# Optimization experiments

Hardware: AMD Instinct MI355X
Metric: run time of the kernel (lower is better)

## Reference

```python
import jax, jax.numpy as jnp
import numpy as np

DIM = 96
HEADS = 6
HEAD_DIM = DIM // HEADS  # 16
WIN = 8
N = WIN * WIN            # 64
C = 4 * DIM              # 384
TABLE = (2 * WIN - 1) ** 2  # 225


def setup_inputs() -> dict:
    key = jax.random.key(0)
    ks = jax.random.split(key, 12)
    B_ = 2048  # num_windows * batch = 1024 * 2
    NW = 1024
    x = jax.random.normal(ks[0], (B_, N, C), dtype=jnp.float32)
    cross_x = jax.random.normal(ks[1], (B_, N, C), dtype=jnp.float32)
    rpi = jax.random.randint(ks[2], (N, N), 0, TABLE)
    mask = jnp.zeros((NW, N, N), dtype=jnp.float32)
    s = 0.02
    Wq = jax.random.normal(ks[3], (C, DIM), dtype=jnp.float32) * s
    bq = jnp.zeros((DIM,), dtype=jnp.float32)
    Wk = jax.random.normal(ks[4], (C, DIM), dtype=jnp.float32) * s
    bk = jnp.zeros((DIM,), dtype=jnp.float32)
    Wv = jax.random.normal(ks[5], (C, C), dtype=jnp.float32) * s
    bv = jnp.zeros((C,), dtype=jnp.float32)
    Wp = jax.random.normal(ks[6], (C, C), dtype=jnp.float32) * s
    bp = jnp.zeros((C,), dtype=jnp.float32)
    rpb_table = jax.random.normal(ks[7], (TABLE, HEADS), dtype=jnp.float32) * 0.02
    return {"x": x, "cross_x": cross_x, "rpi": rpi, "mask": mask,
            "Wq": Wq, "bq": bq, "Wk": Wk, "bk": bk, "Wv": Wv, "bv": bv,
            "Wp": Wp, "bp": bp, "rpb_table": rpb_table}


def reference(x, cross_x, rpi, mask, Wq, bq, Wk, bk, Wv, bv, Wp, bp, rpb_table):
    b_, n, c = x.shape
    scale = HEAD_DIM ** (-0.5)
    # projections: q,k -> dim; v -> c (=4*dim)
    q = (x @ Wq + bq).reshape(b_, n, HEADS, HEAD_DIM).transpose(0, 2, 1, 3)
    k = (cross_x @ Wk + bk).reshape(b_, n, HEADS, HEAD_DIM).transpose(0, 2, 1, 3)
    v = (cross_x @ Wv + bv).reshape(b_, n, HEADS, c // HEADS).transpose(0, 2, 1, 3)
    attn = jnp.einsum('bhnd,bhmd->bhnm', q * scale, k)
    # relative position bias: gather (n*n,) indices -> (n, n, heads) -> (heads, n, n)
    bias = rpb_table[rpi.reshape(-1)].reshape(n, n, HEADS).transpose(2, 0, 1)
    attn = attn + bias[None]
    nw = mask.shape[0]
    attn = attn.reshape(b_ // nw, nw, HEADS, n, n) + mask[None, :, None]
    attn = attn.reshape(b_, HEADS, n, n)
    attn = jax.nn.softmax(attn, axis=-1)
    out = jnp.einsum('bhnm,bhmd->bhnd', attn, v)  # (b_, heads, n, c//heads)
    out = out.transpose(0, 2, 1, 3).reshape(b_, n, c)
    out = out @ Wp + bp
    return out
```

## Files before the change

kernel.cpp:

```cpp
#include <hip/hip_runtime.h>
#include <hip/hip_bf16.h>


typedef __attribute__((ext_vector_type(8))) short short8;
typedef __attribute__((ext_vector_type(4))) float f32x4;

__device__ __forceinline__ f32x4 mfma_b16(short8 a, short8 b, f32x4 c) {
  return __builtin_amdgcn_mfma_f32_16x16x32_bf16(a, b, c, 0, 0, 0);
}

__device__ __forceinline__ unsigned short f2bf(float x) {
  return __builtin_bit_cast(unsigned short, __float2bfloat16(x));
}

__device__ __forceinline__ unsigned pack2(float a, float b) {
  return (unsigned)f2bf(a) | ((unsigned)f2bf(b) << 16);
}

__device__ __forceinline__ int swz48(int c, int r) {
  return (c & ~7) | ((c ^ r) & 7);
}

__device__ __forceinline__ void gl_lds16(const char* g, char* l) {
  __builtin_amdgcn_global_load_lds(
      (const __attribute__((address_space(1))) unsigned int*)g,
      (__attribute__((address_space(3))) unsigned int*)l, 16, 0, 0);
}

__global__ void prep_k(const float* __restrict__ Wq, const float* __restrict__ Wk,
                       const float* __restrict__ Wv, const float* __restrict__ Wp,
                       const float* __restrict__ rpb, const int* __restrict__ rpi,
                       const float* __restrict__ bk, const float* __restrict__ bv,
                       unsigned short* __restrict__ Wq_t, unsigned short* __restrict__ Wkv_t,
                       unsigned short* __restrict__ Wp_t, float* __restrict__ bias6,
                       float* __restrict__ bias_kv) {
  const int T0 = 96 * 384, T1 = 480 * 384, T2 = 384 * 384, T3 = 6 * 4096, T4 = 480;
  int total = T0 + T1 + T2 + T3 + T4;
  for (int i = blockIdx.x * blockDim.x + threadIdx.x; i < total;
       i += gridDim.x * blockDim.x) {
    int r = i;
    if (r < T0) {
      int n = r / 384, k = r % 384;
      Wq_t[r] = f2bf(Wq[k * 96 + n]);
    } else if ((r -= T0) < T1) {
      int n = r / 384, k = r % 384;
      Wkv_t[r] = f2bf(n < 96 ? Wk[k * 96 + n] : Wv[k * 384 + (n - 96)]);
    } else if ((r -= T1) < T2) {
      int n = r / 384, k = r % 384;
      Wp_t[r] = f2bf(Wp[k * 384 + n]);
    } else if ((r -= T2) < T3) {
      int h = r >> 12, ij = r & 4095;
      bias6[r] = rpb[rpi[ij] * 6 + h];
    } else {
      r -= T3;
      bias_kv[r] = (r < 96) ? bk[r] : bv[r - 96];
    }
  }
}

template <int A_MODE, int OUT_MODE, int NX>
__global__ __launch_bounds__(256, 4) void gemm3_k(
    const void* __restrict__ Av, const unsigned short* __restrict__ Bt,
    const float* __restrict__ bias, void* __restrict__ Outv,
    unsigned short* __restrict__ k_out, unsigned short* __restrict__ vt_out) {
  __shared__ char lds[40960];
  constexpr int AB[2] = {0, 8192}, BB[2] = {16384, 28672};
  const int tid = threadIdx.x, lane = tid & 63, wid = tid >> 6;
  const int g = blockIdx.x;
  const int lg_id = (g & 7) * (NX * 256) + (g >> 3);
  const int my = lg_id / NX, nx = lg_id - my * NX;
  const int m0 = my * 64, n0 = nx * 96;
  const int wm = (wid >> 1) * 32, wn = (wid & 1) * 48;
  const int lr = lane & 15, lg = lane >> 4;

  float4 areg[4];
  const int ar = tid >> 2, aq = tid & 3;

  auto a_issue_f32 = [&](int kt) {
    const float* A = (const float*)Av + (size_t)(m0 + ar) * 384 + kt * 64 + aq * 16;
#pragma unroll
    for (int p = 0; p < 4; ++p) areg[p] = *reinterpret_cast<const float4*>(A + p * 4);
  };
  auto a_write_f32 = [&](char* Ab) {
    unsigned pk[8];
#pragma unroll
    for (int p = 0; p < 4; ++p) {
      pk[p * 2]     = pack2(areg[p].x, areg[p].y);
      pk[p * 2 + 1] = pack2(areg[p].z, areg[p].w);
    }
    const int c0 = aq * 2;
    *reinterpret_cast<uint4*>(Ab + ar * 128 + ((c0 ^ (ar & 7)) * 16)) =
        make_uint4(pk[0], pk[1], pk[2], pk[3]);
    *reinterpret_cast<uint4*>(Ab + ar * 128 + (((c0 + 1) ^ (ar & 7)) * 16)) =
        make_uint4(pk[4], pk[5], pk[6], pk[7]);
  };
  auto b_issue = [&](int kt, char* Bb) {
#pragma unroll
    for (int j = 0; j < 3; ++j) {
      const int rb = (wid * 3 + j) * 8;
      const int row = rb + (lane >> 3), c = lane & 7;
      gl_lds16((const char*)Bt + (size_t)(n0 + row) * 768 + kt * 128 +
                   ((c ^ (row & 7)) * 16),
               Bb + rb * 128);
    }
  };

  f32x4 acc[2][3];
#pragma unroll
  for (int i = 0; i < 2; ++i)
#pragma unroll
    for (int j = 0; j < 3; ++j) acc[i][j] = (f32x4){0.f, 0.f, 0.f, 0.f};

  a_issue_f32(0);
  a_write_f32(lds + AB[0]);
  b_issue(0, lds + BB[0]);
  __syncthreads();

  int cur = 0;
  for (int kt = 0; kt < 6; ++kt) {
    char* An = lds + AB[cur ^ 1];
    char* Bn = lds + BB[cur ^ 1];
    if (kt < 5) {
      a_issue_f32(kt + 1);
      b_issue(kt + 1, Bn);
    }
    {
      const char* Ab = lds + AB[cur];
      const char* Bb = lds + BB[cur];
#pragma unroll
      for (int ks = 0; ks < 2; ++ks) {
        short8 a[2], b[3];
#pragma unroll
        for (int mf = 0; mf < 2; ++mf) {
          const int row = wm + mf * 16 + lr;
          a[mf] = *reinterpret_cast<const short8*>(
              Ab + row * 128 + (((ks * 4 + lg) ^ (row & 7)) * 16));
        }
#pragma unroll
        for (int nf = 0; nf < 3; ++nf) {
          const int row = wn + nf * 16 + lr;
          b[nf] = *reinterpret_cast<const short8*>(
              Bb + row * 128 + (((ks * 4 + lg) ^ (row & 7)) * 16));
        }
#pragma unroll
        for (int mf = 0; mf < 2; ++mf)
#pragma unroll
          for (int nf = 0; nf < 3; ++nf)
            acc[mf][nf] = mfma_b16(a[mf], b[nf], acc[mf][nf]);
      }
    }
    if (kt < 5) a_write_f32(An);
    __syncthreads();
    cur ^= 1;
  }

  if (OUT_MODE == 0 || (OUT_MODE == 2 && nx == 0)) {
    unsigned short* dst = (OUT_MODE == 0) ? (unsigned short*)Outv : k_out;
#pragma unroll
    for (int mf = 0; mf < 2; ++mf)
#pragma unroll
      for (int nf = 0; nf < 3; ++nf) {
        const int col = wn + nf * 16 + lr;
        const float bb = bias[col];
#pragma unroll
        for (int r = 0; r < 4; ++r) {
          const int row = wm + mf * 16 + lg * 4 + r;
          *reinterpret_cast<unsigned short*>(lds + row * 208 + col * 2) =
              f2bf(acc[mf][nf][r] + bb);
        }
      }
    __syncthreads();
#pragma unroll
    for (int j = 0; j < 3; ++j) {
      const int Lb = (j * 256 + tid) * 16;
      const int row = Lb / 192, inner = Lb % 192;
      *reinterpret_cast<uint4*>((char*)dst + (size_t)(m0 + row) * 192 + inner) =
          *reinterpret_cast<const uint4*>(lds + row * 208 + inner);
    }
  } else {
#pragma unroll
    for (int mf = 0; mf < 2; ++mf)
#pragma unroll
      for (int nf = 0; nf < 3; ++nf) {
        const int dl = wn + nf * 16 + lr;
        const float bb = bias[n0 + dl];
        const int tok0 = wm + mf * 16 + lg * 4;
        *reinterpret_cast<unsigned*>(lds + dl * 144 + tok0 * 2) =
            pack2(acc[mf][nf][0] + bb, acc[mf][nf][1] + bb);
        *reinterpret_cast<unsigned*>(lds + dl * 144 + tok0 * 2 + 4) =
            pack2(acc[mf][nf][2] + bb, acc[mf][nf][3] + bb);
      }
    __syncthreads();
#pragma unroll
    for (int j = 0; j < 3; ++j) {
      const int Lc = j * 256 + tid;
      const int dl = Lc >> 3, c = Lc & 7;
      *reinterpret_cast<uint4*>((char*)vt_out + (size_t)my * 49152 +
                                (size_t)((nx - 1) * 96 + dl) * 128 +
                                ((c ^ (dl & 7)) << 4)) =
          *reinterpret_cast<const uint4*>(lds + dl * 144 + c * 16);
    }
  }
}

__global__ __launch_bounds__(256, 2) void ap_k(
    const unsigned short* __restrict__ q_buf, const unsigned short* __restrict__ k_buf,
    const unsigned short* __restrict__ vt_buf, const float* __restrict__ bias6,
    const float* __restrict__ mask, const unsigned short* __restrict__ Wp_t,
    const float* __restrict__ bp, float* __restrict__ out) {
  __shared__ char lds[81920];
  const int tid = threadIdx.x, lane = tid & 63, wid = tid >> 6;
  const int lr = lane & 15, lg = lane >> 4;
  const int w = blockIdx.x;

  auto b_issue = [&](int T, char* Bb) {
    const int nc = T / 6, kt = T - nc * 6;
#pragma unroll
    for (int j = 0; j < 3; ++j) {
      const int rb = (wid * 3 + j) * 8;
      const int row = rb + (lane >> 3), c = lane & 7;
      gl_lds16((const char*)Wp_t + (size_t)(nc * 96 + row) * 768 + kt * 128 +
                   ((c ^ (row & 7)) * 16),
               Bb + rb * 128);
    }
  };

  const char* vsrc = (const char*)vt_buf + (size_t)w * 49152;
#pragma unroll
  for (int j = 0; j < 12; ++j) {
    const int off = (wid * 12 + j) * 1024;
    gl_lds16(vsrc + off + lane * 16, lds + off);
  }
  b_issue(0, lds + 57344);
  b_issue(1, lds + 57344 + 12288);
  __syncthreads();

  unsigned stash[48];
  char* Plds = lds + 49152;
  const float* mw = mask + (size_t)(w & 1023) * 4096;
  const int iq = wid * 16 + lr;

  short8 qa_c = {0, 0, 0, 0, 0, 0, 0, 0};
  short8 kf_c[4];
  float4 bm_c[4];
#pragma unroll
  for (int tj = 0; tj < 4; ++tj) kf_c[tj] = (short8){0, 0, 0, 0, 0, 0, 0, 0};
  if (lg < 2) {
    qa_c = *reinterpret_cast<const short8*>(
        q_buf + (size_t)(w * 64 + iq) * 96 + lg * 8);
#pragma unroll
    for (int tj = 0; tj < 4; ++tj)
      kf_c[tj] = *reinterpret_cast<const short8*>(
          k_buf + (size_t)(w * 64 + tj * 16 + lr) * 96 + lg * 8);
  }
#pragma unroll
  for (int tj = 0; tj < 4; ++tj) {
    const int j0 = tj * 16 + lg * 4;
    const float4 bi = *reinterpret_cast<const float4*>(bias6 + iq * 64 + j0);
    const float4 mk = *reinterpret_cast<const float4*>(mw + iq * 64 + j0);
    bm_c[tj] = make_float4(bi.x + mk.x, bi.y + mk.y, bi.z + mk.z, bi.w + mk.w);
  }

#pragma unroll
  for (int h = 0; h < 6; ++h) {
    short8 qa_n = {0, 0, 0, 0, 0, 0, 0, 0};
    short8 kf_n[4];
    float4 bm_n[4];
#pragma unroll
    for (int tj = 0; tj < 4; ++tj) kf_n[tj] = (short8){0, 0, 0, 0, 0, 0, 0, 0};
    if (h < 5) {
      if (lg < 2) {
        qa_n = *reinterpret_cast<const short8*>(
            q_buf + (size_t)(w * 64 + iq) * 96 + (h + 1) * 16 + lg * 8);
#pragma unroll
        for (int tj = 0; tj < 4; ++tj)
          kf_n[tj] = *reinterpret_cast<const short8*>(
              k_buf + (size_t)(w * 64 + tj * 16 + lr) * 96 + (h + 1) * 16 + lg * 8);
      }
#pragma unroll
      for (int tj = 0; tj < 4; ++tj) {
        const int j0 = tj * 16 + lg * 4;
        const float4 bi = *reinterpret_cast<const float4*>(
            bias6 + (h + 1) * 4096 + iq * 64 + j0);
        const float4 mk = *reinterpret_cast<const float4*>(mw + iq * 64 + j0);
        bm_n[tj] = make_float4(bi.x + mk.x, bi.y + mk.y, bi.z + mk.z, bi.w + mk.w);
      }
    }

    float sv[4][4];
#pragma unroll
    for (int tj = 0; tj < 4; ++tj) {
      f32x4 z = {0.f, 0.f, 0.f, 0.f};
      f32x4 s = mfma_b16(kf_c[tj], qa_c, z);
      sv[tj][0] = s[0] * 0.25f + bm_c[tj].x;
      sv[tj][1] = s[1] * 0.25f + bm_c[tj].y;
      sv[tj][2] = s[2] * 0.25f + bm_c[tj].z;
      sv[tj][3] = s[3] * 0.25f + bm_c[tj].w;
    }
    float mx = sv[0][0];
#pragma unroll
    for (int tj = 0; tj < 4; ++tj)
#pragma unroll
      for (int r = 0; r < 4; ++r) mx = fmaxf(mx, sv[tj][r]);
    mx = fmaxf(mx, __shfl_xor(mx, 16));
    mx = fmaxf(mx, __shfl_xor(mx, 32));
    float sum = 0.f;
#pragma unroll
    for (int tj = 0; tj < 4; ++tj)
#pragma unroll
      for (int r = 0; r < 4; ++r) {
        sv[tj][r] = __expf(sv[tj][r] - mx);
        sum += sv[tj][r];
      }
    sum += __shfl_xor(sum, 16);
    sum += __shfl_xor(sum, 32);
    const float inv = 1.0f / sum;
#pragma unroll
    for (int tj = 0; tj < 4; ++tj) {
      const int c = tj * 2 + (lg >> 1);
      uint2 st;
      st.x = pack2(sv[tj][0] * inv, sv[tj][1] * inv);
      st.y = pack2(sv[tj][2] * inv, sv[tj][3] * inv);
      *reinterpret_cast<uint2*>(Plds + iq * 128 + ((c ^ (iq & 7)) << 4) +
                                (lg & 1) * 8) = st;
    }
    short8 pa[2];
#pragma unroll
    for (int ks = 0; ks < 2; ++ks)
      pa[ks] = *reinterpret_cast<const short8*>(
          Plds + iq * 128 + (((ks * 4 + lg) ^ (iq & 7)) << 4));
    __builtin_amdgcn_s_setprio(1);
#pragma unroll
    for (int td = 0; td < 4; ++td) {
      f32x4 o = {0.f, 0.f, 0.f, 0.f};
#pragma unroll
      for (int ks = 0; ks < 2; ++ks) {
        const int d = h * 64 + td * 16 + lr;
        short8 vb = *reinterpret_cast<const short8*>(
            lds + d * 128 + (((ks * 4 + lg) ^ (d & 7)) << 4));
        o = mfma_b16(vb, pa[ks], o);
      }
      stash[h * 8 + td * 2 + 0] = pack2(o[0], o[1]);
      stash[h * 8 + td * 2 + 1] = pack2(o[2], o[3]);
    }
    __builtin_amdgcn_s_setprio(0);
    qa_c = qa_n;
#pragma unroll
    for (int tj = 0; tj < 4; ++tj) {
      kf_c[tj] = kf_n[tj];
      bm_c[tj] = bm_n[tj];
    }
  }
  __syncthreads();

#pragma unroll
  for (int h = 0; h < 6; ++h)
#pragma unroll
    for (int td = 0; td < 4; ++td)
#pragma unroll
      for (int p2 = 0; p2 < 2; ++p2) {
        const int c0 = h * 64 + td * 16 + lg * 4 + p2 * 2;
        *reinterpret_cast<unsigned*>(
            lds + iq * 768 + swz48(c0 >> 3, iq) * 16 + ((c0 * 2) & 15)) =
            stash[h * 8 + td * 2 + p2];
      }
  __syncthreads();

  const int wm = (wid >> 1) * 32, wn = (wid & 1) * 48;
  f32x4 acc[2][3];
#pragma unroll
  for (int i = 0; i < 2; ++i)
#pragma unroll
    for (int j = 0; j < 3; ++j) acc[i][j] = (f32x4){0.f, 0.f, 0.f, 0.f};

#pragma unroll 1
  for (int T = 0; T < 24; ++T) {
    const int nc = T / 6, kt = T - nc * 6;
    if (T >= 1 && T < 23) b_issue(T + 1, lds + 57344 + ((T + 1) & 1) * 12288);
    const char* Bb = lds + 57344 + (T & 1) * 12288;
    __builtin_amdgcn_s_setprio(1);
#pragma unroll
    for (int ks = 0; ks < 2; ++ks) {
      short8 a[2], b[3];
#pragma unroll
      for (int mf = 0; mf < 2; ++mf) {
        const int row = wm + mf * 16 + lr;
        a[mf] = *reinterpret_cast<const short8*>(
            lds + row * 768 + swz48(kt * 8 + ks * 4 + lg, row) * 16);
      }
#pragma unroll
      for (int nf = 0; nf < 3; ++nf) {
        const int row = wn + nf * 16 + lr;
        b[nf] = *reinterpret_cast<const short8*>(
            Bb + row * 128 + (((ks * 4 + lg) ^ (row & 7)) * 16));
      }
#pragma unroll
      for (int mf = 0; mf < 2; ++mf)
#pragma unroll
        for (int nf = 0; nf < 3; ++nf)
          acc[mf][nf] = mfma_b16(a[mf], b[nf], acc[mf][nf]);
    }
    __builtin_amdgcn_s_setprio(0);
    if (kt == 5) {
#pragma unroll
      for (int mf = 0; mf < 2; ++mf)
#pragma unroll
        for (int nf = 0; nf < 3; ++nf) {
          const int col = nc * 96 + wn + nf * 16 + lr;
          const float bb = bp[col];
#pragma unroll
          for (int r = 0; r < 4; ++r) {
            const int row = wm + mf * 16 + lg * 4 + r;
            out[(size_t)(w * 64 + row) * 384 + col] = acc[mf][nf][r] + bb;
          }
          acc[mf][nf] = (f32x4){0.f, 0.f, 0.f, 0.f};
        }
    }
    __syncthreads();
  }
}

extern "C" void kernel_launch(void* const* d_in, const int* in_sizes, int n_in,
                              void* d_out, int out_size, void* d_ws, size_t ws_size,
                              hipStream_t stream) {
  const float* x    = (const float*)d_in[0];
  const float* cx   = (const float*)d_in[1];
  const int*   rpi  = (const int*)d_in[2];
  const float* mask = (const float*)d_in[3];
  const float* Wq   = (const float*)d_in[4];
  const float* bq   = (const float*)d_in[5];
  const float* Wk   = (const float*)d_in[6];
  const float* bk   = (const float*)d_in[7];
  const float* Wv   = (const float*)d_in[8];
  const float* bv   = (const float*)d_in[9];
  const float* Wp   = (const float*)d_in[10];
  const float* bp   = (const float*)d_in[11];
  const float* rpb  = (const float*)d_in[12];

  char* ws = (char*)d_ws;
  unsigned short* Wq_t   = (unsigned short*)(ws + 0);
  unsigned short* Wkv_t  = (unsigned short*)(ws + 73728);
  unsigned short* Wp_t   = (unsigned short*)(ws + 442368);
  float*          bias6  = (float*)(ws + 737280);
  float*          biaskv = (float*)(ws + 835584);
  const size_t MB = 1u << 20;
  unsigned short* q_buf  = (unsigned short*)(ws + MB);
  unsigned short* k_buf  = (unsigned short*)(ws + MB + 25165824u);
  unsigned short* vt_buf = (unsigned short*)(ws + MB + 50331648u);

  prep_k<<<256, 256, 0, stream>>>(Wq, Wk, Wv, Wp, rpb, rpi, bk, bv,
                                  Wq_t, Wkv_t, Wp_t, bias6, biaskv);
  gemm3_k<0, 0, 1><<<2048, 256, 0, stream>>>(x, Wq_t, bq, q_buf, nullptr, nullptr);
  gemm3_k<0, 2, 5><<<10240, 256, 0, stream>>>(cx, Wkv_t, biaskv, nullptr, k_buf, vt_buf);
  ap_k<<<2048, 256, 0, stream>>>(q_buf, k_buf, vt_buf, bias6, mask, Wp_t, bp,
                                 (float*)d_out);
}
```

Before: 352.1 us.

## Replace syncthreads with split-counter waits and per-wave B tile loads

Each wave now loads exactly the B rows it consumes (its 48-column half) instead of a shared third. That lets the double-buffered GEMM loops in gemm3_k and ap_k replace full __syncthreads with explicit partial vmcnt waits plus an LDS-only barrier. The goal is to let the next tile's global loads stay in flight across the barrier rather than draining all memory counters each iteration. In exchange, each B row is loaded by two waves, doubling L2 traffic for weights, and correctness now relies on hand-tuned vmcnt counts.

```diff
diff --git a/kernel.cpp b/kernel.cpp
--- a/kernel.cpp
+++ b/kernel.cpp
@@ -26,6 +26,12 @@
       (const __attribute__((address_space(1))) unsigned int*)g,
       (__attribute__((address_space(3))) unsigned int*)l, 16, 0, 0);
 }
+
+#define RAWBAR                          \
+  asm volatile("s_waitcnt lgkmcnt(0)" ::: "memory"); \
+  __builtin_amdgcn_sched_barrier(0);    \
+  __builtin_amdgcn_s_barrier();         \
+  __builtin_amdgcn_sched_barrier(0)
 
 __global__ void prep_k(const float* __restrict__ Wq, const float* __restrict__ Wk,
                        const float* __restrict__ Wv, const float* __restrict__ Wp,
@@ -58,7 +64,7 @@
   }
 }
 
-template <int A_MODE, int OUT_MODE, int NX>
+template <int OUT_MODE, int NX>
 __global__ __launch_bounds__(256, 4) void gemm3_k(
     const void* __restrict__ Av, const unsigned short* __restrict__ Bt,
     const float* __restrict__ bias, void* __restrict__ Outv,
@@ -76,12 +82,12 @@
   float4 areg[4];
   const int ar = tid >> 2, aq = tid & 3;
 
-  auto a_issue_f32 = [&](int kt) {
+  auto a_issue = [&](int kt) {
     const float* A = (const float*)Av + (size_t)(m0 + ar) * 384 + kt * 64 + aq * 16;
 #pragma unroll
     for (int p = 0; p < 4; ++p) areg[p] = *reinterpret_cast<const float4*>(A + p * 4);
   };
-  auto a_write_f32 = [&](char* Ab) {
+  auto a_write = [&](char* Ab) {
     unsigned pk[8];
 #pragma unroll
     for (int p = 0; p < 4; ++p) {
@@ -96,8 +102,8 @@
   };
   auto b_issue = [&](int kt, char* Bb) {
 #pragma unroll
-    for (int j = 0; j < 3; ++j) {
-      const int rb = (wid * 3 + j) * 8;
+    for (int j = 0; j < 6; ++j) {
+      const int rb = wn + j * 8;
       const int row = rb + (lane >> 3), c = lane & 7;
       gl_lds16((const char*)Bt + (size_t)(n0 + row) * 768 + kt * 128 +
                    ((c ^ (row & 7)) * 16),
@@ -111,19 +117,22 @@
 #pragma unroll
     for (int j = 0; j < 3; ++j) acc[i][j] = (f32x4){0.f, 0.f, 0.f, 0.f};
 
-  a_issue_f32(0);
-  a_write_f32(lds + AB[0]);
+  a_issue(0);
   b_issue(0, lds + BB[0]);
-  __syncthreads();
+  a_write(lds + AB[0]);
+  RAWBAR;
 
   int cur = 0;
+#pragma unroll 1
   for (int kt = 0; kt < 6; ++kt) {
-    char* An = lds + AB[cur ^ 1];
-    char* Bn = lds + BB[cur ^ 1];
     if (kt < 5) {
-      a_issue_f32(kt + 1);
-      b_issue(kt + 1, Bn);
-    }
+      a_issue(kt + 1);
+      b_issue(kt + 1, lds + BB[cur ^ 1]);
+      asm volatile("s_waitcnt vmcnt(10)" ::: "memory");
+    } else {
+      asm volatile("s_waitcnt vmcnt(0)" ::: "memory");
+    }
+    __builtin_amdgcn_sched_barrier(0);
     {
       const char* Ab = lds + AB[cur];
       const char* Bb = lds + BB[cur];
@@ -149,11 +158,12 @@
             acc[mf][nf] = mfma_b16(a[mf], b[nf], acc[mf][nf]);
       }
     }
-    if (kt < 5) a_write_f32(An);
-    __syncthreads();
+    if (kt < 5) a_write(lds + AB[cur ^ 1]);
+    RAWBAR;
     cur ^= 1;
   }
 
+  __syncthreads();
   if (OUT_MODE == 0 || (OUT_MODE == 2 && nx == 0)) {
     unsigned short* dst = (OUT_MODE == 0) ? (unsigned short*)Outv : k_out;
 #pragma unroll
@@ -212,12 +222,13 @@
   const int tid = threadIdx.x, lane = tid & 63, wid = tid >> 6;
   const int lr = lane & 15, lg = lane >> 4;
   const int w = blockIdx.x;
+  const int wn = (wid & 1) * 48;
 
   auto b_issue = [&](int T, char* Bb) {
     const int nc = T / 6, kt = T - nc * 6;
 #pragma unroll
-    for (int j = 0; j < 3; ++j) {
-      const int rb = (wid * 3 + j) * 8;
+    for (int j = 0; j < 6; ++j) {
+      const int rb = wn + j * 8;
       const int row = rb + (lane >> 3), c = lane & 7;
       gl_lds16((const char*)Wp_t + (size_t)(nc * 96 + row) * 768 + kt * 128 +
                    ((c ^ (row & 7)) * 16),
@@ -232,7 +243,6 @@
     gl_lds16(vsrc + off + lane * 16, lds + off);
   }
   b_issue(0, lds + 57344);
-  b_issue(1, lds + 57344 + 12288);
   __syncthreads();
 
   unsigned stash[48];
@@ -366,7 +376,7 @@
       }
   __syncthreads();
 
-  const int wm = (wid >> 1) * 32, wn = (wid & 1) * 48;
+  const int wm = (wid >> 1) * 32;
   f32x4 acc[2][3];
 #pragma unroll
   for (int i = 0; i < 2; ++i)
@@ -376,7 +386,15 @@
 #pragma unroll 1
   for (int T = 0; T < 24; ++T) {
     const int nc = T / 6, kt = T - nc * 6;
-    if (T >= 1 && T < 23) b_issue(T + 1, lds + 57344 + ((T + 1) & 1) * 12288);
+    if (T < 23) b_issue(T + 1, lds + 57344 + ((T + 1) & 1) * 12288);
+    if (T == 23) {
+      asm volatile("s_waitcnt vmcnt(0)" ::: "memory");
+    } else if (T > 0 && kt == 0) {
+      asm volatile("s_waitcnt vmcnt(30)" ::: "memory");
+    } else {
+      asm volatile("s_waitcnt vmcnt(6)" ::: "memory");
+    }
+    __builtin_amdgcn_sched_barrier(0);
     const char* Bb = lds + 57344 + (T & 1) * 12288;
     __builtin_amdgcn_s_setprio(1);
 #pragma unroll
@@ -416,7 +434,7 @@
           acc[mf][nf] = (f32x4){0.f, 0.f, 0.f, 0.f};
         }
     }
-    __syncthreads();
+    RAWBAR;
   }
 }
 
@@ -450,8 +468,8 @@
 
   prep_k<<<256, 256, 0, stream>>>(Wq, Wk, Wv, Wp, rpb, rpi, bk, bv,
                                   Wq_t, Wkv_t, Wp_t, bias6, biaskv);
-  gemm3_k<0, 0, 1><<<2048, 256, 0, stream>>>(x, Wq_t, bq, q_buf, nullptr, nullptr);
-  gemm3_k<0, 2, 5><<<10240, 256, 0, stream>>>(cx, Wkv_t, biaskv, nullptr, k_buf, vt_buf);
+  gemm3_k<0, 1><<<2048, 256, 0, stream>>>(x, Wq_t, bq, q_buf, nullptr, nullptr);
+  gemm3_k<2, 5><<<10240, 256, 0, stream>>>(cx, Wkv_t, biaskv, nullptr, k_buf, vt_buf);
   ap_k<<<2048, 256, 0, stream>>>(q_buf, k_buf, vt_buf, bias6, mask, Wp_t, bp,
                                  (float*)d_out);
 }
```

New measurement: 363.7 us. +3.3%, slower.
